# Performance work log

Measured on AMD Instinct MI355X. Metric: run time of the kernel, lower is better.

## Reference

```python
import jax, jax.numpy as jnp
import numpy as np

B, H, W, Z = 4, 256, 256, 64
ITERATIONS = 8
EPSILON = 1e-06
CENTER = 6.0  # 7-point Laplacian diagonal


def _stencil(x):
    # x: [B, H, W, Z]; zero (Dirichlet) boundaries via padded shifts
    west = jnp.pad(x[:, :, :-1, :], ((0, 0), (0, 0), (1, 0), (0, 0)))
    east = jnp.pad(x[:, :, 1:, :], ((0, 0), (0, 0), (0, 1), (0, 0)))
    north = jnp.pad(x[:, :-1, :, :], ((0, 0), (1, 0), (0, 0), (0, 0)))
    south = jnp.pad(x[:, 1:, :, :], ((0, 0), (0, 1), (0, 0), (0, 0)))
    bottom = jnp.pad(x[:, :, :, :-1], ((0, 0), (0, 0), (0, 0), (1, 0)))
    top = jnp.pad(x[:, :, :, 1:], ((0, 0), (0, 0), (0, 0), (0, 1)))
    return CENTER * x - west - east - south - north - bottom - top


def _dot(a, b):
    # per-sample dot product, keepdims for scalar broadcast
    return jnp.sum(a * b, axis=(1, 2, 3), keepdims=True)


def setup_inputs() -> dict:
    key = jax.random.key(0)
    k1, k2, k3 = jax.random.split(key, 3)
    shape = (B, H, W, Z)
    return {
        "x": jax.random.normal(k1, shape, dtype=jnp.float32),
        "b": jax.random.normal(k2, shape, dtype=jnp.float32),
        "reference_sol": jax.random.normal(k3, shape, dtype=jnp.float32),
    }


def reference(x, b, reference_sol):
    r = b - _stencil(x)
    p = r
    rho = _dot(r, r)

    def body(carry, _):
        x, r, p, rho = carry
        w = _stencil(p)
        eta = _dot(p, w)
        alpha = rho / (eta + EPSILON)
        x = x + alpha * p
        r = r - alpha * w
        rho_next = _dot(r, r)
        beta = rho_next / (rho + EPSILON)
        p = r + beta * p
        return (x, r, p, rho_next), None

    (x, r, p, rho), _ = jax.lax.scan(body, (x, r, p, rho), None, length=ITERATIONS)

    diff = x - reference_sol
    loss = jnp.mean(diff * diff)
    max_error = jnp.max(jnp.abs(diff))
    residual_norm_sq = jnp.mean(rho)
    return (loss, x, max_error, residual_norm_sq)
```

## Files before the change

### kernel.cpp

```cpp
#include <hip/hip_runtime.h>

#define B_ 4
#define H_ 256
#define W_ 256
#define Z_ 64
#define NB_ (H_*W_*Z_)
#define N_  (B_*NB_)
#define ITER_ 8
#define EPS_ 1e-6f
#define SLOTS_ 64

#define RHO_OFF   0
#define ETA_OFF   ((ITER_+1)*B_*SLOTS_)
#define LOSS_OFF  (ETA_OFF + ITER_*B_*SLOTS_)
#define MAXE_OFF  (LOSS_OFF + SLOTS_)
#define SCAL_FLOATS (MAXE_OFF + SLOTS_)

struct F8 { float4 a, b; };

__device__ __forceinline__ float wsum(float v){
  v += __shfl_xor(v,32); v += __shfl_xor(v,16); v += __shfl_xor(v,8);
  v += __shfl_xor(v,4);  v += __shfl_xor(v,2);  v += __shfl_xor(v,1);
  return v;
}
__device__ __forceinline__ float wmaxr(float v){
  v = fmaxf(v,__shfl_xor(v,32)); v = fmaxf(v,__shfl_xor(v,16));
  v = fmaxf(v,__shfl_xor(v,8));  v = fmaxf(v,__shfl_xor(v,4));
  v = fmaxf(v,__shfl_xor(v,2));  v = fmaxf(v,__shfl_xor(v,1));
  return v;
}
__device__ __forceinline__ float read_sum(const float* s){
  return wsum(s[threadIdx.x & 63]);
}
__device__ __forceinline__ void block_atomic_sum(float v, float* dst, float* lds){
  v = wsum(v);
  int wid = threadIdx.x >> 6, lane = threadIdx.x & 63;
  if (lane == 0) lds[wid] = v;
  __syncthreads();
  if (threadIdx.x == 0) atomicAdd(dst, lds[0]+lds[1]+lds[2]+lds[3]);
}

__device__ __forceinline__ float4 ld4(const float* p){ return *(const float4*)p; }

__device__ __forceinline__ void sten_core(const F8& c, const F8& wm, const F8& wp,
                                          const F8& hm, const F8& hp,
                                          float zl, float zr, F8& st)
{
  st.a.x = 6.f*c.a.x - wm.a.x - wp.a.x - hm.a.x - hp.a.x - zl     - c.a.y;
  st.a.y = 6.f*c.a.y - wm.a.y - wp.a.y - hm.a.y - hp.a.y - c.a.x  - c.a.z;
  st.a.z = 6.f*c.a.z - wm.a.z - wp.a.z - hm.a.z - hp.a.z - c.a.y  - c.a.w;
  st.a.w = 6.f*c.a.w - wm.a.w - wp.a.w - hm.a.w - hp.a.w - c.a.z  - c.b.x;
  st.b.x = 6.f*c.b.x - wm.b.x - wp.b.x - hm.b.x - hp.b.x - c.a.w  - c.b.y;
  st.b.y = 6.f*c.b.y - wm.b.y - wp.b.y - hm.b.y - hp.b.y - c.b.x  - c.b.z;
  st.b.z = 6.f*c.b.z - wm.b.z - wp.b.z - hm.b.z - hp.b.z - c.b.y  - c.b.w;
  st.b.w = 6.f*c.b.w - wm.b.w - wp.b.w - hm.b.w - hp.b.w - c.b.z  - zr;
}

__device__ __forceinline__ void stencil1(const float* __restrict__ a, int base,
                                         int w, int h, int zc, F8& c, F8& st)
{
  c.a = ld4(a+base); c.b = ld4(a+base+4);
  F8 zero; zero.a = make_float4(0,0,0,0); zero.b = zero.a;
  F8 wm = zero, wp = zero, hm = zero, hp = zero;
  if (w > 0)    { wm.a = ld4(a+base-Z_);    wm.b = ld4(a+base-Z_+4); }
  if (w < W_-1) { wp.a = ld4(a+base+Z_);    wp.b = ld4(a+base+Z_+4); }
  if (h > 0)    { hm.a = ld4(a+base-W_*Z_); hm.b = ld4(a+base-W_*Z_+4); }
  if (h < H_-1) { hp.a = ld4(a+base+W_*Z_); hp.b = ld4(a+base+W_*Z_+4); }
  float zl = (zc > 0) ? a[base-1] : 0.f;
  float zr = (zc < 7) ? a[base+8] : 0.f;
  sten_core(c, wm, wp, hm, hp, zl, zr, st);
}

__device__ __forceinline__ F8 comb8(const float* r, const float* p, float beta, int idx){
  F8 o;
  float4 ra = ld4(r+idx), rb = ld4(r+idx+4);
  float4 pa = ld4(p+idx), pb = ld4(p+idx+4);
  o.a.x = ra.x + beta*pa.x; o.a.y = ra.y + beta*pa.y;
  o.a.z = ra.z + beta*pa.z; o.a.w = ra.w + beta*pa.w;
  o.b.x = rb.x + beta*pb.x; o.b.y = rb.y + beta*pb.y;
  o.b.z = rb.z + beta*pb.z; o.b.w = rb.w + beta*pb.w;
  return o;
}
__device__ __forceinline__ void stencil2(const float* __restrict__ r,
                                         const float* __restrict__ p, float beta,
                                         int base, int w, int h, int zc,
                                         F8& c, F8& st)
{
  c = comb8(r,p,beta,base);
  F8 zero; zero.a = make_float4(0,0,0,0); zero.b = zero.a;
  F8 wm = zero, wp = zero, hm = zero, hp = zero;
  if (w > 0)    wm = comb8(r,p,beta,base-Z_);
  if (w < W_-1) wp = comb8(r,p,beta,base+Z_);
  if (h > 0)    hm = comb8(r,p,beta,base-W_*Z_);
  if (h < H_-1) hp = comb8(r,p,beta,base+W_*Z_);
  float zl = (zc > 0) ? r[base-1] + beta*p[base-1] : 0.f;
  float zr = (zc < 7) ? r[base+8] + beta*p[base+8] : 0.f;
  sten_core(c, wm, wp, hm, hp, zl, zr, st);
}

#define IDX_SETUP \
  const int zc = threadIdx.x & 7; \
  const int wl = threadIdx.x >> 3; \
  const int w  = blockIdx.x*32 + wl; \
  const int h  = blockIdx.y; \
  const int bb = blockIdx.z; \
  const int base = ((bb*H_ + h)*W_ + w)*Z_ + zc*8; \
  const int flat = (blockIdx.z*gridDim.y + blockIdx.y)*gridDim.x + blockIdx.x; \
  const int slot = flat & (SLOTS_-1);

__global__ __launch_bounds__(256) void k_init(const float* __restrict__ x,
                                              const float* __restrict__ b,
                                              float* __restrict__ r,
                                              float* scal)
{
  __shared__ float lds[4];
  IDX_SETUP
  F8 c, st;
  stencil1(x, base, w, h, zc, c, st);
  float4 b0 = ld4(b+base), b1 = ld4(b+base+4);
  F8 rv;
  rv.a = make_float4(b0.x-st.a.x, b0.y-st.a.y, b0.z-st.a.z, b0.w-st.a.w);
  rv.b = make_float4(b1.x-st.b.x, b1.y-st.b.y, b1.z-st.b.z, b1.w-st.b.w);
  *(float4*)(r+base)   = rv.a;
  *(float4*)(r+base+4) = rv.b;
  float rho = rv.a.x*rv.a.x + rv.a.y*rv.a.y + rv.a.z*rv.a.z + rv.a.w*rv.a.w
            + rv.b.x*rv.b.x + rv.b.y*rv.b.y + rv.b.z*rv.b.z + rv.b.w*rv.b.w;
  block_atomic_sum(rho, scal + RHO_OFF + (0*B_+bb)*SLOTS_ + slot, lds);
}

__global__ __launch_bounds__(256) void k_a0(const float* __restrict__ r,
                                            float* __restrict__ pnew,
                                            float* scal)
{
  __shared__ float lds[4];
  IDX_SETUP
  F8 c, st;
  stencil1(r, base, w, h, zc, c, st);
  *(float4*)(pnew+base)   = c.a;
  *(float4*)(pnew+base+4) = c.b;
  float eta = c.a.x*st.a.x + c.a.y*st.a.y + c.a.z*st.a.z + c.a.w*st.a.w
            + c.b.x*st.b.x + c.b.y*st.b.y + c.b.z*st.b.z + c.b.w*st.b.w;
  block_atomic_sum(eta, scal + ETA_OFF + (0*B_+bb)*SLOTS_ + slot, lds);
}

__global__ __launch_bounds__(256) void k_a(const float* __restrict__ r,
                                           const float* __restrict__ pold,
                                           float* __restrict__ pnew,
                                           float* scal, int it)
{
  __shared__ float lds[4];
  IDX_SETUP
  float num = read_sum(scal + RHO_OFF + (it*B_+bb)*SLOTS_);
  float den = read_sum(scal + RHO_OFF + ((it-1)*B_+bb)*SLOTS_);
  float beta = num / (den + EPS_);
  F8 c, st;
  stencil2(r, pold, beta, base, w, h, zc, c, st);
  *(float4*)(pnew+base)   = c.a;
  *(float4*)(pnew+base+4) = c.b;
  float eta = c.a.x*st.a.x + c.a.y*st.a.y + c.a.z*st.a.z + c.a.w*st.a.w
            + c.b.x*st.b.x + c.b.y*st.b.y + c.b.z*st.b.z + c.b.w*st.b.w;
  block_atomic_sum(eta, scal + ETA_OFF + (it*B_+bb)*SLOTS_ + slot, lds);
}

__global__ __launch_bounds__(256) void k_b(float* __restrict__ x,
                                           float* __restrict__ r,
                                           const float* __restrict__ p,
                                           float* scal, int it)
{
  __shared__ float lds[4];
  IDX_SETUP
  float num = read_sum(scal + RHO_OFF + (it*B_+bb)*SLOTS_);
  float den = read_sum(scal + ETA_OFF + (it*B_+bb)*SLOTS_);
  float alpha = num / (den + EPS_);
  F8 c, st;
  stencil1(p, base, w, h, zc, c, st);
  float4 x0 = ld4(x+base), x1 = ld4(x+base+4);
  x0.x += alpha*c.a.x; x0.y += alpha*c.a.y; x0.z += alpha*c.a.z; x0.w += alpha*c.a.w;
  x1.x += alpha*c.b.x; x1.y += alpha*c.b.y; x1.z += alpha*c.b.z; x1.w += alpha*c.b.w;
  *(float4*)(x+base)   = x0;
  *(float4*)(x+base+4) = x1;
  float4 r0 = ld4(r+base), r1 = ld4(r+base+4);
  r0.x -= alpha*st.a.x; r0.y -= alpha*st.a.y; r0.z -= alpha*st.a.z; r0.w -= alpha*st.a.w;
  r1.x -= alpha*st.b.x; r1.y -= alpha*st.b.y; r1.z -= alpha*st.b.z; r1.w -= alpha*st.b.w;
  *(float4*)(r+base)   = r0;
  *(float4*)(r+base+4) = r1;
  float rho = r0.x*r0.x + r0.y*r0.y + r0.z*r0.z + r0.w*r0.w
            + r1.x*r1.x + r1.y*r1.y + r1.z*r1.z + r1.w*r1.w;
  block_atomic_sum(rho, scal + RHO_OFF + ((it+1)*B_+bb)*SLOTS_ + slot, lds);
}

__global__ __launch_bounds__(256) void k_b_fin(const float* __restrict__ x,
                                               const float* __restrict__ r,
                                               const float* __restrict__ p,
                                               const float* __restrict__ ref,
                                               float* __restrict__ out,
                                               float* scal, int it)
{
  __shared__ float xs[2048];
  __shared__ float lds[12];
  IDX_SETUP
  float num = read_sum(scal + RHO_OFF + (it*B_+bb)*SLOTS_);
  float den = read_sum(scal + ETA_OFF + (it*B_+bb)*SLOTS_);
  float alpha = num / (den + EPS_);
  F8 c, st;
  stencil1(p, base, w, h, zc, c, st);
  float4 x0 = ld4(x+base), x1 = ld4(x+base+4);
  x0.x += alpha*c.a.x; x0.y += alpha*c.a.y; x0.z += alpha*c.a.z; x0.w += alpha*c.a.w;
  x1.x += alpha*c.b.x; x1.y += alpha*c.b.y; x1.z += alpha*c.b.z; x1.w += alpha*c.b.w;
  float4 r0 = ld4(r+base), r1 = ld4(r+base+4);
  r0.x -= alpha*st.a.x; r0.y -= alpha*st.a.y; r0.z -= alpha*st.a.z; r0.w -= alpha*st.a.w;
  r1.x -= alpha*st.b.x; r1.y -= alpha*st.b.y; r1.z -= alpha*st.b.z; r1.w -= alpha*st.b.w;
  float rho = r0.x*r0.x + r0.y*r0.y + r0.z*r0.z + r0.w*r0.w
            + r1.x*r1.x + r1.y*r1.y + r1.z*r1.z + r1.w*r1.w;

  const int t = threadIdx.x;
  xs[t*8+0] = x0.x; xs[t*8+1] = x0.y; xs[t*8+2] = x0.z; xs[t*8+3] = x0.w;
  xs[t*8+4] = x1.x; xs[t*8+5] = x1.y; xs[t*8+6] = x1.z; xs[t*8+7] = x1.w;

  float4 f0 = ld4(ref+base), f1 = ld4(ref+base+4);
  float d0 = x0.x-f0.x, d1 = x0.y-f0.y, d2 = x0.z-f0.z, d3 = x0.w-f0.w;
  float d4 = x1.x-f1.x, d5 = x1.y-f1.y, d6 = x1.z-f1.z, d7 = x1.w-f1.w;
  float loss = d0*d0+d1*d1+d2*d2+d3*d3+d4*d4+d5*d5+d6*d6+d7*d7;
  float me = fmaxf(fmaxf(fmaxf(fabsf(d0),fabsf(d1)),fmaxf(fabsf(d2),fabsf(d3))),
                   fmaxf(fmaxf(fabsf(d4),fabsf(d5)),fmaxf(fabsf(d6),fabsf(d7))));

  float rs = wsum(rho), ls = wsum(loss), ms = wmaxr(me);
  int wid = t >> 6, lane = t & 63;
  if (lane == 0) { lds[wid] = rs; lds[4+wid] = ls; lds[8+wid] = ms; }
  __syncthreads();
  if (t == 0) {
    atomicAdd(scal + RHO_OFF + ((it+1)*B_+bb)*SLOTS_ + slot, lds[0]+lds[1]+lds[2]+lds[3]);
    atomicAdd(scal + LOSS_OFF + slot, lds[4]+lds[5]+lds[6]+lds[7]);
    float bm = fmaxf(fmaxf(lds[8],lds[9]), fmaxf(lds[10],lds[11]));
    atomicMax((unsigned int*)(scal + MAXE_OFF) + slot, __float_as_uint(bm));
  }

  const int S = flat * 2048;
  #pragma unroll
  for (int c2 = 0; c2 < 2; ++c2) {
    int q = t + 256*c2;
    if (q < 511) {
      float4 v = make_float4(xs[3+4*q], xs[4+4*q], xs[5+4*q], xs[6+4*q]);
      *(float4*)(out + S + 4 + 4*q) = v;
    } else if (q == 511) {
      out[S+1] = xs[0]; out[S+2] = xs[1]; out[S+3] = xs[2];
      out[S+2048] = xs[2047];
    }
  }
}

__global__ __launch_bounds__(64) void k_scal(const float* scal, float* out)
{
  int lane = threadIdx.x;
  float loss = wsum(scal[LOSS_OFF + lane]);
  float me   = wmaxr(__uint_as_float(((const unsigned int*)scal)[MAXE_OFF + lane]));
  float rho_sum = 0.f;
  for (int bb = 0; bb < B_; ++bb)
    rho_sum += wsum(scal[RHO_OFF + (ITER_*B_+bb)*SLOTS_ + lane]);
  if (lane == 0) {
    out[0]      = loss / (float)N_;
    out[1+N_]   = me;
    out[2+N_]   = rho_sum / (float)B_;
  }
}

extern "C" void kernel_launch(void* const* d_in, const int* in_sizes, int n_in,
                              void* d_out, int out_size, void* d_ws, size_t ws_size,
                              hipStream_t stream) {
  float* x         = (float*)d_in[0];
  const float* b   = (const float*)d_in[1];
  const float* ref = (const float*)d_in[2];
  float* out       = (float*)d_out;

  float* r  = (float*)d_ws;
  float* p0 = r + N_;
  float* p1;
  float* scal;
  size_t need3 = ((size_t)3*N_ + SCAL_FLOATS) * sizeof(float);
  if (ws_size >= need3) {
    p1   = p0 + N_;
    scal = p1 + N_;
  } else {
    p1   = (float*)d_out;
    scal = p0 + N_;
  }

  (void)hipMemsetAsync(scal, 0, SCAL_FLOATS*sizeof(float), stream);

  dim3 grid(W_/32, H_, B_), blk(256);
  k_init<<<grid, blk, 0, stream>>>(x, b, r, scal);

  float* pa = p1;
  float* pb = p0;
  for (int it = 0; it < ITER_; ++it) {
    if (it == 0)
      k_a0<<<grid, blk, 0, stream>>>(r, pa, scal);
    else
      k_a<<<grid, blk, 0, stream>>>(r, pb, pa, scal, it);
    if (it < ITER_-1)
      k_b<<<grid, blk, 0, stream>>>(x, r, pa, scal, it);
    else
      k_b_fin<<<grid, blk, 0, stream>>>(x, r, pa, ref, out, scal, it);
    float* t = pa; pa = pb; pb = t;
  }

  k_scal<<<1, 64, 0, stream>>>(scal, out);
}
```

Measured before the change: 1.097 ms.

## Process two H rows per thread, shuffle Z halos, skip initial p copy

Each thread now computes two adjacent H rows, so each row's centre values also serve as the other row's vertical neighbour. This cuts H-direction halo reloads and halves the grid. Z-direction halo values now come from wavefront shuffles instead of scalar global loads. The first iteration no longer writes p (p0 equals r), and r is double-buffered so the first k_b reads r as p; the final k_b_fin stays on one row per thread.

```diff
diff --git a/kernel.cpp b/kernel.cpp
--- a/kernel.cpp
+++ b/kernel.cpp
@@ -42,9 +42,203 @@
 
 __device__ __forceinline__ float4 ld4(const float* p){ return *(const float4*)p; }
 
-__device__ __forceinline__ void sten_core(const F8& c, const F8& wm, const F8& wp,
-                                          const F8& hm, const F8& hp,
-                                          float zl, float zr, F8& st)
+__device__ __forceinline__ void sub8(F8& s, const F8& n){
+  s.a.x-=n.a.x; s.a.y-=n.a.y; s.a.z-=n.a.z; s.a.w-=n.a.w;
+  s.b.x-=n.b.x; s.b.y-=n.b.y; s.b.z-=n.b.z; s.b.w-=n.b.w;
+}
+
+__device__ __forceinline__ void zcore(const F8& c, int zc, F8& st){
+  float zl = __shfl_up(c.b.w, 1);
+  float zr = __shfl_down(c.a.x, 1);
+  zl = (zc > 0) ? zl : 0.f;
+  zr = (zc < 7) ? zr : 0.f;
+  st.a.x = 6.f*c.a.x - zl    - c.a.y;
+  st.a.y = 6.f*c.a.y - c.a.x - c.a.z;
+  st.a.z = 6.f*c.a.z - c.a.y - c.a.w;
+  st.a.w = 6.f*c.a.w - c.a.z - c.b.x;
+  st.b.x = 6.f*c.b.x - c.a.w - c.b.y;
+  st.b.y = 6.f*c.b.y - c.b.x - c.b.z;
+  st.b.z = 6.f*c.b.z - c.b.y - c.b.w;
+  st.b.w = 6.f*c.b.w - c.b.z - zr;
+}
+
+__device__ __forceinline__ void stencil1_2(const float* __restrict__ a, int base0,
+                                           int w, int h0, int zc,
+                                           F8& c0, F8& c1, F8& st0, F8& st1)
+{
+  const int base1 = base0 + W_*Z_;
+  c0.a = ld4(a+base0); c0.b = ld4(a+base0+4);
+  c1.a = ld4(a+base1); c1.b = ld4(a+base1+4);
+  zcore(c0, zc, st0);
+  zcore(c1, zc, st1);
+  F8 t;
+  if (w > 0)    { t.a = ld4(a+base0-Z_); t.b = ld4(a+base0-Z_+4); sub8(st0,t);
+                  t.a = ld4(a+base1-Z_); t.b = ld4(a+base1-Z_+4); sub8(st1,t); }
+  if (w < W_-1) { t.a = ld4(a+base0+Z_); t.b = ld4(a+base0+Z_+4); sub8(st0,t);
+                  t.a = ld4(a+base1+Z_); t.b = ld4(a+base1+Z_+4); sub8(st1,t); }
+  if (h0 > 0)   { t.a = ld4(a+base0-W_*Z_); t.b = ld4(a+base0-W_*Z_+4); sub8(st0,t); }
+  sub8(st0, c1);
+  sub8(st1, c0);
+  if (h0 < H_-2){ t.a = ld4(a+base1+W_*Z_); t.b = ld4(a+base1+W_*Z_+4); sub8(st1,t); }
+}
+
+__device__ __forceinline__ F8 comb8(const float* r, const float* p, float beta, int idx){
+  F8 o;
+  float4 ra = ld4(r+idx), rb = ld4(r+idx+4);
+  float4 pa = ld4(p+idx), pb = ld4(p+idx+4);
+  o.a.x = ra.x + beta*pa.x; o.a.y = ra.y + beta*pa.y;
+  o.a.z = ra.z + beta*pa.z; o.a.w = ra.w + beta*pa.w;
+  o.b.x = rb.x + beta*pb.x; o.b.y = rb.y + beta*pb.y;
+  o.b.z = rb.z + beta*pb.z; o.b.w = rb.w + beta*pb.w;
+  return o;
+}
+__device__ __forceinline__ void stencil2_2(const float* __restrict__ r,
+                                           const float* __restrict__ p, float beta,
+                                           int base0, int w, int h0, int zc,
+                                           F8& c0, F8& c1, F8& st0, F8& st1)
+{
+  const int base1 = base0 + W_*Z_;
+  c0 = comb8(r,p,beta,base0);
+  c1 = comb8(r,p,beta,base1);
+  zcore(c0, zc, st0);
+  zcore(c1, zc, st1);
+  if (w > 0)    { sub8(st0, comb8(r,p,beta,base0-Z_));
+                  sub8(st1, comb8(r,p,beta,base1-Z_)); }
+  if (w < W_-1) { sub8(st0, comb8(r,p,beta,base0+Z_));
+                  sub8(st1, comb8(r,p,beta,base1+Z_)); }
+  if (h0 > 0)   sub8(st0, comb8(r,p,beta,base0-W_*Z_));
+  sub8(st0, c1);
+  sub8(st1, c0);
+  if (h0 < H_-2) sub8(st1, comb8(r,p,beta,base1+W_*Z_));
+}
+
+__device__ __forceinline__ float dot8(const F8& a, const F8& b){
+  return a.a.x*b.a.x + a.a.y*b.a.y + a.a.z*b.a.z + a.a.w*b.a.w
+       + a.b.x*b.b.x + a.b.y*b.b.y + a.b.z*b.b.z + a.b.w*b.b.w;
+}
+
+#define IDX2_SETUP \
+  const int zc = threadIdx.x & 7; \
+  const int wl = threadIdx.x >> 3; \
+  const int w  = blockIdx.x*32 + wl; \
+  const int h0 = blockIdx.y*2; \
+  const int bb = blockIdx.z; \
+  const int base0 = ((bb*H_ + h0)*W_ + w)*Z_ + zc*8; \
+  const int flat = (blockIdx.z*gridDim.y + blockIdx.y)*gridDim.x + blockIdx.x; \
+  const int slot = flat & (SLOTS_-1);
+
+__global__ __launch_bounds__(256) void k_init2(const float* __restrict__ x,
+                                               const float* __restrict__ b,
+                                               float* __restrict__ r,
+                                               float* scal)
+{
+  __shared__ float lds[4];
+  IDX2_SETUP
+  const int base1 = base0 + W_*Z_;
+  F8 c0,c1,st0,st1;
+  stencil1_2(x, base0, w, h0, zc, c0, c1, st0, st1);
+  float4 b0 = ld4(b+base0), b1 = ld4(b+base0+4);
+  float4 b2 = ld4(b+base1), b3 = ld4(b+base1+4);
+  F8 rv0, rv1;
+  rv0.a = make_float4(b0.x-st0.a.x, b0.y-st0.a.y, b0.z-st0.a.z, b0.w-st0.a.w);
+  rv0.b = make_float4(b1.x-st0.b.x, b1.y-st0.b.y, b1.z-st0.b.z, b1.w-st0.b.w);
+  rv1.a = make_float4(b2.x-st1.a.x, b2.y-st1.a.y, b2.z-st1.a.z, b2.w-st1.a.w);
+  rv1.b = make_float4(b3.x-st1.b.x, b3.y-st1.b.y, b3.z-st1.b.z, b3.w-st1.b.w);
+  *(float4*)(r+base0)   = rv0.a;
+  *(float4*)(r+base0+4) = rv0.b;
+  *(float4*)(r+base1)   = rv1.a;
+  *(float4*)(r+base1+4) = rv1.b;
+  block_atomic_sum(dot8(rv0,rv0)+dot8(rv1,rv1),
+                   scal + RHO_OFF + (0*B_+bb)*SLOTS_ + slot, lds);
+}
+
+__global__ __launch_bounds__(256) void k_a0_2(const float* __restrict__ r,
+                                              float* __restrict__ pnew,
+                                              float* scal)
+{
+  __shared__ float lds[4];
+  IDX2_SETUP
+  const int base1 = base0 + W_*Z_;
+  F8 c0,c1,st0,st1;
+  stencil1_2(r, base0, w, h0, zc, c0, c1, st0, st1);
+  if (pnew) {
+    *(float4*)(pnew+base0)   = c0.a; *(float4*)(pnew+base0+4) = c0.b;
+    *(float4*)(pnew+base1)   = c1.a; *(float4*)(pnew+base1+4) = c1.b;
+  }
+  block_atomic_sum(dot8(c0,st0)+dot8(c1,st1),
+                   scal + ETA_OFF + (0*B_+bb)*SLOTS_ + slot, lds);
+}
+
+__global__ __launch_bounds__(256) void k_a2(const float* __restrict__ r,
+                                            const float* __restrict__ pold,
+                                            float* __restrict__ pnew,
+                                            float* scal, int it)
+{
+  __shared__ float lds[4];
+  IDX2_SETUP
+  const int base1 = base0 + W_*Z_;
+  float num = read_sum(scal + RHO_OFF + (it*B_+bb)*SLOTS_);
+  float den = read_sum(scal + RHO_OFF + ((it-1)*B_+bb)*SLOTS_);
+  float beta = num / (den + EPS_);
+  F8 c0,c1,st0,st1;
+  stencil2_2(r, pold, beta, base0, w, h0, zc, c0, c1, st0, st1);
+  *(float4*)(pnew+base0)   = c0.a;
+  *(float4*)(pnew+base0+4) = c0.b;
+  *(float4*)(pnew+base1)   = c1.a;
+  *(float4*)(pnew+base1+4) = c1.b;
+  block_atomic_sum(dot8(c0,st0)+dot8(c1,st1),
+                   scal + ETA_OFF + (it*B_+bb)*SLOTS_ + slot, lds);
+}
+
+__global__ __launch_bounds__(256) void k_b2(float* __restrict__ x,
+                                            const float* r_in,
+                                            float* r_out,
+                                            const float* p,
+                                            float* scal, int it)
+{
+  __shared__ float lds[4];
+  IDX2_SETUP
+  const int base1 = base0 + W_*Z_;
+  float num = read_sum(scal + RHO_OFF + (it*B_+bb)*SLOTS_);
+  float den = read_sum(scal + ETA_OFF + (it*B_+bb)*SLOTS_);
+  float alpha = num / (den + EPS_);
+  F8 c0,c1,st0,st1;
+  stencil1_2(p, base0, w, h0, zc, c0, c1, st0, st1);
+  float rho = 0.f;
+  {
+    float4 x0 = ld4(x+base0), x1 = ld4(x+base0+4);
+    x0.x += alpha*c0.a.x; x0.y += alpha*c0.a.y; x0.z += alpha*c0.a.z; x0.w += alpha*c0.a.w;
+    x1.x += alpha*c0.b.x; x1.y += alpha*c0.b.y; x1.z += alpha*c0.b.z; x1.w += alpha*c0.b.w;
+    *(float4*)(x+base0)   = x0;
+    *(float4*)(x+base0+4) = x1;
+    float4 r0 = ld4(r_in+base0), r1 = ld4(r_in+base0+4);
+    r0.x -= alpha*st0.a.x; r0.y -= alpha*st0.a.y; r0.z -= alpha*st0.a.z; r0.w -= alpha*st0.a.w;
+    r1.x -= alpha*st0.b.x; r1.y -= alpha*st0.b.y; r1.z -= alpha*st0.b.z; r1.w -= alpha*st0.b.w;
+    *(float4*)(r_out+base0)   = r0;
+    *(float4*)(r_out+base0+4) = r1;
+    rho += r0.x*r0.x + r0.y*r0.y + r0.z*r0.z + r0.w*r0.w
+         + r1.x*r1.x + r1.y*r1.y + r1.z*r1.z + r1.w*r1.w;
+  }
+  {
+    float4 x0 = ld4(x+base1), x1 = ld4(x+base1+4);
+    x0.x += alpha*c1.a.x; x0.y += alpha*c1.a.y; x0.z += alpha*c1.a.z; x0.w += alpha*c1.a.w;
+    x1.x += alpha*c1.b.x; x1.y += alpha*c1.b.y; x1.z += alpha*c1.b.z; x1.w += alpha*c1.b.w;
+    *(float4*)(x+base1)   = x0;
+    *(float4*)(x+base1+4) = x1;
+    float4 r0 = ld4(r_in+base1), r1 = ld4(r_in+base1+4);
+    r0.x -= alpha*st1.a.x; r0.y -= alpha*st1.a.y; r0.z -= alpha*st1.a.z; r0.w -= alpha*st1.a.w;
+    r1.x -= alpha*st1.b.x; r1.y -= alpha*st1.b.y; r1.z -= alpha*st1.b.z; r1.w -= alpha*st1.b.w;
+    *(float4*)(r_out+base1)   = r0;
+    *(float4*)(r_out+base1+4) = r1;
+    rho += r0.x*r0.x + r0.y*r0.y + r0.z*r0.z + r0.w*r0.w
+         + r1.x*r1.x + r1.y*r1.y + r1.z*r1.z + r1.w*r1.w;
+  }
+  block_atomic_sum(rho, scal + RHO_OFF + ((it+1)*B_+bb)*SLOTS_ + slot, lds);
+}
+
+__device__ __forceinline__ void sten_core_o(const F8& c, const F8& wm, const F8& wp,
+                                            const F8& hm, const F8& hp,
+                                            float zl, float zr, F8& st)
 {
   st.a.x = 6.f*c.a.x - wm.a.x - wp.a.x - hm.a.x - hp.a.x - zl     - c.a.y;
   st.a.y = 6.f*c.a.y - wm.a.y - wp.a.y - hm.a.y - hp.a.y - c.a.x  - c.a.z;
@@ -55,9 +249,8 @@
   st.b.z = 6.f*c.b.z - wm.b.z - wp.b.z - hm.b.z - hp.b.z - c.b.y  - c.b.w;
   st.b.w = 6.f*c.b.w - wm.b.w - wp.b.w - hm.b.w - hp.b.w - c.b.z  - zr;
 }
-
-__device__ __forceinline__ void stencil1(const float* __restrict__ a, int base,
-                                         int w, int h, int zc, F8& c, F8& st)
+__device__ __forceinline__ void stencil1_o(const float* __restrict__ a, int base,
+                                           int w, int h, int zc, F8& c, F8& st)
 {
   c.a = ld4(a+base); c.b = ld4(a+base+4);
   F8 zero; zero.a = make_float4(0,0,0,0); zero.b = zero.a;
@@ -68,125 +261,7 @@
   if (h < H_-1) { hp.a = ld4(a+base+W_*Z_); hp.b = ld4(a+base+W_*Z_+4); }
   float zl = (zc > 0) ? a[base-1] : 0.f;
   float zr = (zc < 7) ? a[base+8] : 0.f;
-  sten_core(c, wm, wp, hm, hp, zl, zr, st);
-}
-
-__device__ __forceinline__ F8 comb8(const float* r, const float* p, float beta, int idx){
-  F8 o;
-  float4 ra = ld4(r+idx), rb = ld4(r+idx+4);
-  float4 pa = ld4(p+idx), pb = ld4(p+idx+4);
-  o.a.x = ra.x + beta*pa.x; o.a.y = ra.y + beta*pa.y;
-  o.a.z = ra.z + beta*pa.z; o.a.w = ra.w + beta*pa.w;
-  o.b.x = rb.x + beta*pb.x; o.b.y = rb.y + beta*pb.y;
-  o.b.z = rb.z + beta*pb.z; o.b.w = rb.w + beta*pb.w;
-  return o;
-}
-__device__ __forceinline__ void stencil2(const float* __restrict__ r,
-                                         const float* __restrict__ p, float beta,
-                                         int base, int w, int h, int zc,
-                                         F8& c, F8& st)
-{
-  c = comb8(r,p,beta,base);
-  F8 zero; zero.a = make_float4(0,0,0,0); zero.b = zero.a;
-  F8 wm = zero, wp = zero, hm = zero, hp = zero;
-  if (w > 0)    wm = comb8(r,p,beta,base-Z_);
-  if (w < W_-1) wp = comb8(r,p,beta,base+Z_);
-  if (h > 0)    hm = comb8(r,p,beta,base-W_*Z_);
-  if (h < H_-1) hp = comb8(r,p,beta,base+W_*Z_);
-  float zl = (zc > 0) ? r[base-1] + beta*p[base-1] : 0.f;
-  float zr = (zc < 7) ? r[base+8] + beta*p[base+8] : 0.f;
-  sten_core(c, wm, wp, hm, hp, zl, zr, st);
-}
-
-#define IDX_SETUP \
-  const int zc = threadIdx.x & 7; \
-  const int wl = threadIdx.x >> 3; \
-  const int w  = blockIdx.x*32 + wl; \
-  const int h  = blockIdx.y; \
-  const int bb = blockIdx.z; \
-  const int base = ((bb*H_ + h)*W_ + w)*Z_ + zc*8; \
-  const int flat = (blockIdx.z*gridDim.y + blockIdx.y)*gridDim.x + blockIdx.x; \
-  const int slot = flat & (SLOTS_-1);
-
-__global__ __launch_bounds__(256) void k_init(const float* __restrict__ x,
-                                              const float* __restrict__ b,
-                                              float* __restrict__ r,
-                                              float* scal)
-{
-  __shared__ float lds[4];
-  IDX_SETUP
-  F8 c, st;
-  stencil1(x, base, w, h, zc, c, st);
-  float4 b0 = ld4(b+base), b1 = ld4(b+base+4);
-  F8 rv;
-  rv.a = make_float4(b0.x-st.a.x, b0.y-st.a.y, b0.z-st.a.z, b0.w-st.a.w);
-  rv.b = make_float4(b1.x-st.b.x, b1.y-st.b.y, b1.z-st.b.z, b1.w-st.b.w);
-  *(float4*)(r+base)   = rv.a;
-  *(float4*)(r+base+4) = rv.b;
-  float rho = rv.a.x*rv.a.x + rv.a.y*rv.a.y + rv.a.z*rv.a.z + rv.a.w*rv.a.w
-            + rv.b.x*rv.b.x + rv.b.y*rv.b.y + rv.b.z*rv.b.z + rv.b.w*rv.b.w;
-  block_atomic_sum(rho, scal + RHO_OFF + (0*B_+bb)*SLOTS_ + slot, lds);
-}
-
-__global__ __launch_bounds__(256) void k_a0(const float* __restrict__ r,
-                                            float* __restrict__ pnew,
-                                            float* scal)
-{
-  __shared__ float lds[4];
-  IDX_SETUP
-  F8 c, st;
-  stencil1(r, base, w, h, zc, c, st);
-  *(float4*)(pnew+base)   = c.a;
-  *(float4*)(pnew+base+4) = c.b;
-  float eta = c.a.x*st.a.x + c.a.y*st.a.y + c.a.z*st.a.z + c.a.w*st.a.w
-            + c.b.x*st.b.x + c.b.y*st.b.y + c.b.z*st.b.z + c.b.w*st.b.w;
-  block_atomic_sum(eta, scal + ETA_OFF + (0*B_+bb)*SLOTS_ + slot, lds);
-}
-
-__global__ __launch_bounds__(256) void k_a(const float* __restrict__ r,
-                                           const float* __restrict__ pold,
-                                           float* __restrict__ pnew,
-                                           float* scal, int it)
-{
-  __shared__ float lds[4];
-  IDX_SETUP
-  float num = read_sum(scal + RHO_OFF + (it*B_+bb)*SLOTS_);
-  float den = read_sum(scal + RHO_OFF + ((it-1)*B_+bb)*SLOTS_);
-  float beta = num / (den + EPS_);
-  F8 c, st;
-  stencil2(r, pold, beta, base, w, h, zc, c, st);
-  *(float4*)(pnew+base)   = c.a;
-  *(float4*)(pnew+base+4) = c.b;
-  float eta = c.a.x*st.a.x + c.a.y*st.a.y + c.a.z*st.a.z + c.a.w*st.a.w
-            + c.b.x*st.b.x + c.b.y*st.b.y + c.b.z*st.b.z + c.b.w*st.b.w;
-  block_atomic_sum(eta, scal + ETA_OFF + (it*B_+bb)*SLOTS_ + slot, lds);
-}
-
-__global__ __launch_bounds__(256) void k_b(float* __restrict__ x,
-                                           float* __restrict__ r,
-                                           const float* __restrict__ p,
-                                           float* scal, int it)
-{
-  __shared__ float lds[4];
-  IDX_SETUP
-  float num = read_sum(scal + RHO_OFF + (it*B_+bb)*SLOTS_);
-  float den = read_sum(scal + ETA_OFF + (it*B_+bb)*SLOTS_);
-  float alpha = num / (den + EPS_);
-  F8 c, st;
-  stencil1(p, base, w, h, zc, c, st);
-  float4 x0 = ld4(x+base), x1 = ld4(x+base+4);
-  x0.x += alpha*c.a.x; x0.y += alpha*c.a.y; x0.z += alpha*c.a.z; x0.w += alpha*c.a.w;
-  x1.x += alpha*c.b.x; x1.y += alpha*c.b.y; x1.z += alpha*c.b.z; x1.w += alpha*c.b.w;
-  *(float4*)(x+base)   = x0;
-  *(float4*)(x+base+4) = x1;
-  float4 r0 = ld4(r+base), r1 = ld4(r+base+4);
-  r0.x -= alpha*st.a.x; r0.y -= alpha*st.a.y; r0.z -= alpha*st.a.z; r0.w -= alpha*st.a.w;
-  r1.x -= alpha*st.b.x; r1.y -= alpha*st.b.y; r1.z -= alpha*st.b.z; r1.w -= alpha*st.b.w;
-  *(float4*)(r+base)   = r0;
-  *(float4*)(r+base+4) = r1;
-  float rho = r0.x*r0.x + r0.y*r0.y + r0.z*r0.z + r0.w*r0.w
-            + r1.x*r1.x + r1.y*r1.y + r1.z*r1.z + r1.w*r1.w;
-  block_atomic_sum(rho, scal + RHO_OFF + ((it+1)*B_+bb)*SLOTS_ + slot, lds);
+  sten_core_o(c, wm, wp, hm, hp, zl, zr, st);
 }
 
 __global__ __launch_bounds__(256) void k_b_fin(const float* __restrict__ x,
@@ -198,12 +273,19 @@
 {
   __shared__ float xs[2048];
   __shared__ float lds[12];
-  IDX_SETUP
+  const int zc = threadIdx.x & 7;
+  const int wl = threadIdx.x >> 3;
+  const int w  = blockIdx.x*32 + wl;
+  const int h  = blockIdx.y;
+  const int bb = blockIdx.z;
+  const int base = ((bb*H_ + h)*W_ + w)*Z_ + zc*8;
+  const int flat = (blockIdx.z*gridDim.y + blockIdx.y)*gridDim.x + blockIdx.x;
+  const int slot = flat & (SLOTS_-1);
   float num = read_sum(scal + RHO_OFF + (it*B_+bb)*SLOTS_);
   float den = read_sum(scal + ETA_OFF + (it*B_+bb)*SLOTS_);
   float alpha = num / (den + EPS_);
   F8 c, st;
-  stencil1(p, base, w, h, zc, c, st);
+  stencil1_o(p, base, w, h, zc, c, st);
   float4 x0 = ld4(x+base), x1 = ld4(x+base+4);
   x0.x += alpha*c.a.x; x0.y += alpha*c.a.y; x0.z += alpha*c.a.z; x0.w += alpha*c.a.w;
   x1.x += alpha*c.b.x; x1.y += alpha*c.b.y; x1.z += alpha*c.b.z; x1.w += alpha*c.b.w;
@@ -268,41 +350,52 @@
                               void* d_out, int out_size, void* d_ws, size_t ws_size,
                               hipStream_t stream) {
   float* x         = (float*)d_in[0];
-  const float* b   = (const float*)d_in[1];
+  const float* bv  = (const float*)d_in[1];
   const float* ref = (const float*)d_in[2];
   float* out       = (float*)d_out;
-
-  float* r  = (float*)d_ws;
-  float* p0 = r + N_;
-  float* p1;
-  float* scal;
-  size_t need3 = ((size_t)3*N_ + SCAL_FLOATS) * sizeof(float);
-  if (ws_size >= need3) {
-    p1   = p0 + N_;
-    scal = p1 + N_;
+  float* ws        = (float*)d_ws;
+
+  dim3 g2(W_/32, H_/2, B_), gF(W_/32, H_, B_), blk(256);
+  bool fast = ws_size >= ((size_t)3*N_ + SCAL_FLOATS) * sizeof(float);
+
+  if (fast) {
+    float* R0 = ws;
+    float* R1 = ws + N_;
+    float* P0 = ws + 2*(size_t)N_;
+    float* P1 = out;
+    float* scal = ws + 3*(size_t)N_;
+    (void)hipMemsetAsync(scal, 0, SCAL_FLOATS*sizeof(float), stream);
+
+    k_init2<<<g2, blk, 0, stream>>>(x, bv, R0, scal);
+    k_a0_2 <<<g2, blk, 0, stream>>>(R0, nullptr, scal);
+    k_b2   <<<g2, blk, 0, stream>>>(x, R0, R1, R0, scal, 0);
+    float* pa = P0; float* pb = R0;
+    for (int it = 1; it < ITER_; ++it) {
+      k_a2<<<g2, blk, 0, stream>>>(R1, pb, pa, scal, it);
+      if (it < ITER_-1)
+        k_b2<<<g2, blk, 0, stream>>>(x, R1, R1, pa, scal, it);
+      else
+        k_b_fin<<<gF, blk, 0, stream>>>(x, R1, pa, ref, out, scal, it);
+      pb = pa; pa = (pa == P0) ? P1 : P0;
+    }
   } else {
-    p1   = (float*)d_out;
-    scal = p0 + N_;
-  }
-
-  (void)hipMemsetAsync(scal, 0, SCAL_FLOATS*sizeof(float), stream);
-
-  dim3 grid(W_/32, H_, B_), blk(256);
-  k_init<<<grid, blk, 0, stream>>>(x, b, r, scal);
-
-  float* pa = p1;
-  float* pb = p0;
-  for (int it = 0; it < ITER_; ++it) {
-    if (it == 0)
-      k_a0<<<grid, blk, 0, stream>>>(r, pa, scal);
-    else
-      k_a<<<grid, blk, 0, stream>>>(r, pb, pa, scal, it);
-    if (it < ITER_-1)
-      k_b<<<grid, blk, 0, stream>>>(x, r, pa, scal, it);
-    else
-      k_b_fin<<<grid, blk, 0, stream>>>(x, r, pa, ref, out, scal, it);
-    float* t = pa; pa = pb; pb = t;
-  }
-
-  k_scal<<<1, 64, 0, stream>>>(scal, out);
-}
+    float* r    = ws;
+    float* p0w  = ws + N_;
+    float* scal = ws + 2*(size_t)N_;
+    (void)hipMemsetAsync(scal, 0, SCAL_FLOATS*sizeof(float), stream);
+
+    k_init2<<<g2, blk, 0, stream>>>(x, bv, r, scal);
+    k_a0_2 <<<g2, blk, 0, stream>>>(r, out, scal);
+    k_b2   <<<g2, blk, 0, stream>>>(x, r, r, out, scal, 0);
+    float* pa = p0w; float* pb = out;
+    for (int it = 1; it < ITER_; ++it) {
+      k_a2<<<g2, blk, 0, stream>>>(r, pb, pa, scal, it);
+      if (it < ITER_-1)
+        k_b2<<<g2, blk, 0, stream>>>(x, r, r, pa, scal, it);
+      else
+        k_b_fin<<<gF, blk, 0, stream>>>(x, r, pa, ref, out, scal, it);
+      pb = pa; pa = (pa == p0w) ? out : p0w;
+    }
+  }
+  k_scal<<<1, 64, 0, stream>>>((fast ? ws + 3*(size_t)N_ : ws + 2*(size_t)N_), out);
+}
```

Measured after the change: 972.7 us. 11.3% less time.
